# Optimization experiments

Hardware: AMD Instinct MI355X
Metric: run time of the kernel (lower is better)

Reference implementation:

```python
import jax, jax.numpy as jnp
import numpy as np
import math

DIM = 1024
NUM_HEADS = 16
QUANTUM_HEADS = 2
HEAD_DIM = DIM // NUM_HEADS          # 64
TRAD_HEADS = NUM_HEADS - QUANTUM_HEADS  # 14
B, S = 1, 1024
STEPS = 2048
LN_EPS = 1e-5


def setup_inputs() -> dict:
    key = jax.random.key(0)
    ks = jax.random.split(key, 10)
    hd2 = 2 * HEAD_DIM
    return {
        "x": jax.random.normal(ks[0], (B, S, DIM), jnp.float32),
        # to_quantum_state: Linear(head_dim -> 2*head_dim) + LayerNorm + Tanh (shared across quantum heads)
        "qs_W": jax.random.normal(ks[1], (hd2, HEAD_DIM), jnp.float32) / math.sqrt(HEAD_DIM),
        "qs_b": jnp.zeros((hd2,), jnp.float32),
        "ln_g": jnp.ones((hd2,), jnp.float32),
        "ln_b": jnp.zeros((hd2,), jnp.float32),
        # per-quantum-head scalars
        "q_freq": jax.random.normal(ks[2], (QUANTUM_HEADS,), jnp.float32) * 0.02,
        "q_shift": jax.random.normal(ks[3], (QUANTUM_HEADS,), jnp.float32) * 0.02,
        # traditional head projections (no bias)
        "Wq": jax.random.normal(ks[4], (TRAD_HEADS * HEAD_DIM, DIM), jnp.float32) / math.sqrt(DIM),
        "Wk": jax.random.normal(ks[5], (TRAD_HEADS * HEAD_DIM, DIM), jnp.float32) / math.sqrt(DIM),
        "Wv": jax.random.normal(ks[6], (TRAD_HEADS * HEAD_DIM, DIM), jnp.float32) / math.sqrt(DIM),
        # output projection (with bias)
        "Wo": jax.random.normal(ks[7], (DIM, DIM), jnp.float32) / math.sqrt(DIM),
        "bo": jnp.zeros((DIM,), jnp.float32),
    }


def _layernorm(h, g, b):
    mu = jnp.mean(h, axis=-1, keepdims=True)
    var = jnp.mean(jnp.square(h - mu), axis=-1, keepdims=True)
    return (h - mu) * jax.lax.rsqrt(var + LN_EPS) * g + b


def _forward(x, qs_W, qs_b, ln_g, ln_b, q_freq, q_shift, Wq, Wk, Wv, Wo, bo):
    cos_table = jnp.cos(jnp.linspace(0.0, 2.0 * math.pi, STEPS).astype(jnp.float32))
    scale = 1.0 / math.sqrt(HEAD_DIM)
    two_pi = 2.0 * math.pi

    outs = []
    # ---- quantum heads (small fixed loop over structurally distinct heads) ----
    for h in range(QUANTUM_HEADS):
        xh = x[..., h * HEAD_DIM:(h + 1) * HEAD_DIM]          # (B,S,hd)
        qs = jnp.tanh(_layernorm(xh @ qs_W.T + qs_b, ln_g, ln_b))  # (B,S,2hd)
        amp, phase = jnp.split(qs, 2, axis=-1)                 # each (B,S,hd)
        # per (query pos i, key pos j, feature d) phase difference
        pd = (phase[:, :, None, :] - phase[:, None, :, :]) * q_freq[h] + q_shift[h]  # (B,S,S,hd)
        idx = jnp.floor(jnp.mod(pd / two_pi * STEPS, STEPS)).astype(jnp.int32)
        interf = cos_table[idx]                                # lookup-table gather, (B,S,S,hd)
        attn = jnp.einsum('bid,bjd,bijd->bij', amp, amp, interf) * scale
        attn = jax.nn.softmax(attn, axis=-1)
        outs.append(attn @ xh)                                 # (B,S,hd), values are the raw head slice

    # ---- traditional heads: standard multi-head attention ----
    q = (x @ Wq.T).reshape(B, S, TRAD_HEADS, HEAD_DIM)
    k = (x @ Wk.T).reshape(B, S, TRAD_HEADS, HEAD_DIM)
    v = (x @ Wv.T).reshape(B, S, TRAD_HEADS, HEAD_DIM)
    scores = jnp.einsum('bqhd,bkhd->bhqk', q, k) * scale       # (B,Ht,S,S)
    probs = jax.nn.softmax(scores, axis=-1)
    trad = jnp.einsum('bhqk,bkhd->bqhd', probs, v).reshape(B, S, TRAD_HEADS * HEAD_DIM)
    outs.append(trad)

    out = jnp.concatenate(outs, axis=-1)                       # (B,S,DIM)
    return out @ Wo.T + bo


def reference(x, qs_W, qs_b, ln_g, ln_b, q_freq, q_shift, Wq, Wk, Wv, Wo, bo):
    return _forward(x, qs_W, qs_b, ln_g, ln_b, q_freq, q_shift, Wq, Wk, Wv, Wo, bo)
```

## Files before the change

### kernel.cpp

```cpp
#include <hip/hip_runtime.h>
#include <hip/hip_bf16.h>
#include <math.h>

#define DIMX 1024
#define SEQ  1024
#define HD   64
#define QH   2
#define TH   14
#define QKVN 2688
#define LN_EPS 1e-5f
#define NSPLIT 4

typedef __bf16 bf16x8 __attribute__((ext_vector_type(8)));
typedef float  f32x4  __attribute__((ext_vector_type(4)));
typedef unsigned short u16x8 __attribute__((ext_vector_type(8)));

__device__ inline unsigned short f2b_rne(float f) {
  unsigned int u = __float_as_uint(f);
  unsigned int r = (u + 0x7FFF + ((u >> 16) & 1)) >> 16;
  return (unsigned short)r;
}

__device__ inline float waveRedSum(float v) {
  #pragma unroll
  for (int off = 32; off; off >>= 1) v += __shfl_xor(v, off, 64);
  return v;
}

__global__ __launch_bounds__(256) void k_f2b_all(
    const float* __restrict__ x, const float* __restrict__ wq,
    const float* __restrict__ wk, const float* __restrict__ wv,
    const float* __restrict__ wo,
    unsigned short* __restrict__ x_bf, unsigned short* __restrict__ wqkv_bf,
    unsigned short* __restrict__ wo_bf) {
  long i = ((long)blockIdx.x * 256 + threadIdx.x) * 4;
  float4 v;
  unsigned short* dst;
  if (i < 1048576) {
    v = *reinterpret_cast<const float4*>(x + i);
    dst = x_bf + i;
  } else if (i < 3801088) {
    long j = i - 1048576;
    const float* s = (j < 917504) ? wq + j
                   : (j < 1835008) ? wk + (j - 917504)
                                   : wv + (j - 1835008);
    v = *reinterpret_cast<const float4*>(s);
    dst = wqkv_bf + j;
  } else {
    long j = i - 3801088;
    v = *reinterpret_cast<const float4*>(wo + j);
    dst = wo_bf + j;
  }
  ushort4 o;
  o.x = f2b_rne(v.x); o.y = f2b_rne(v.y); o.z = f2b_rne(v.z); o.w = f2b_rne(v.w);
  *reinterpret_cast<ushort4*>(dst) = o;
}

__global__ __launch_bounds__(128) void k_qprep(
    const float* __restrict__ x, const float* __restrict__ qsW,
    const float* __restrict__ qsb, const float* __restrict__ lng,
    const float* __restrict__ lnb, const float* __restrict__ qfreq,
    const float* __restrict__ qshift,
    unsigned short* __restrict__ qcs, unsigned short* __restrict__ kcs) {
  int b = blockIdx.x; int h = b >> 10; int i = b & 1023;
  int o = threadIdx.x;
  __shared__ float xrow[HD];
  __shared__ float red[4];
  __shared__ float qsv[128];
  if (o < HD) xrow[o] = x[i * DIMX + h * HD + o];
  __syncthreads();
  float s = qsb[o];
  #pragma unroll
  for (int d = 0; d < HD; d += 4) {
    float4 w = *reinterpret_cast<const float4*>(qsW + o * HD + d);
    float4 xv = *reinterpret_cast<const float4*>(&xrow[d]);
    s += xv.x * w.x + xv.y * w.y + xv.z * w.z + xv.w * w.w;
  }
  int wid = o >> 6, lane = o & 63;
  float ws = waveRedSum(s);
  if (lane == 0) red[wid] = ws;
  __syncthreads();
  float mu = (red[0] + red[1]) * (1.0f / 128.0f);
  float dv = s - mu;
  float ws2 = waveRedSum(dv * dv);
  if (lane == 0) red[2 + wid] = ws2;
  __syncthreads();
  float var = (red[2] + red[3]) * (1.0f / 128.0f);
  float y = dv * rsqrtf(var + LN_EPS) * lng[o] + lnb[o];
  qsv[o] = tanhf(y);
  __syncthreads();
  float freq = qfreq[h], shift = qshift[h];
  size_t base = ((size_t)h * 1024 + i) * 128;
  if (o < HD) {
    float amp = qsv[o];
    float a = qsv[64 + o] * freq + shift;
    float sn, cs;
    __sincosf(a, &sn, &cs);
    qcs[base + o]      = f2b_rne(amp * cs);
    qcs[base + 64 + o] = f2b_rne(amp * sn);
  } else {
    int d = o - 64;
    float amp = qsv[d];
    float bAng = qsv[64 + d] * freq;
    float sn, cs;
    __sincosf(bAng, &sn, &cs);
    kcs[base + d]      = f2b_rne(amp * cs);
    kcs[base + 64 + d] = f2b_rne(amp * sn);
  }
}

__global__ __launch_bounds__(256) void k_tr64(const unsigned short* __restrict__ src, int ld,
                                              int col0, unsigned short* __restrict__ dst) {
  int h = blockIdx.y, kv0 = blockIdx.x * 64;
  int t = threadIdx.x;
  __shared__ unsigned short tile[64][72];
  #pragma unroll
  for (int pass = 0; pass < 2; ++pass) {
    int s = pass * 256 + t;
    int r = s >> 3, c8 = (s & 7) * 8;
    u16x8 v = *reinterpret_cast<const u16x8*>(src + (size_t)(kv0 + r) * ld + col0 + h * 64 + c8);
    *reinterpret_cast<u16x8*>(&tile[r][c8]) = v;
  }
  __syncthreads();
  #pragma unroll
  for (int pass = 0; pass < 2; ++pass) {
    int s = pass * 256 + t;
    int d = s >> 3, k8 = (s & 7) * 8;
    u16x8 o;
    #pragma unroll
    for (int j = 0; j < 8; ++j) o[j] = tile[k8 + j][d];
    *reinterpret_cast<u16x8*>(dst + (size_t)h * 65536 + (size_t)d * 1024 + kv0 + k8) = o;
  }
}

template <int DQK>
__global__ __launch_bounds__(256) void k_fattn(
    const unsigned short* __restrict__ Qb, long q_hstep, int ldq,
    const unsigned short* __restrict__ Kb, long k_hstep, int ldk,
    const unsigned short* __restrict__ Vtb, long v_hstep, int lh0,
    float* __restrict__ pout, float* __restrict__ pml) {
  const int LQ = DQK + 8;
  const int KREG = DQK / 32;
  __shared__ unsigned short Qs[64 * LQ];
  __shared__ unsigned short Ks[2][64 * LQ];
  __shared__ unsigned short Vs[2][64 * 72];
  __shared__ unsigned short Ps[64 * 72];
  int h = blockIdx.y;
  int q0 = blockIdx.x * 64;
  int split = blockIdx.z;
  int kv0 = split * 256;
  int t = threadIdx.x, lane = t & 63, w = t >> 6;
  int g = lane >> 4, li = lane & 15;
  const unsigned short* Qp = Qb + (size_t)h * q_hstep;
  const unsigned short* Kp = Kb + (size_t)h * k_hstep;
  const unsigned short* Vp = Vtb + (size_t)h * v_hstep;

  #pragma unroll
  for (int i = 0; i < DQK / 32; ++i) {
    int s = i * 64 + lane;
    int r = s / (DQK / 8), c8 = (s % (DQK / 8)) * 8;
    u16x8 v = *reinterpret_cast<const u16x8*>(Qp + (size_t)(q0 + w * 16 + r) * ldq + c8);
    *reinterpret_cast<u16x8*>(&Qs[(w * 16 + r) * LQ + c8]) = v;
  }

  u16x8 kreg[KREG], vreg[2];
  auto loadKV = [&](int tile) {
    int j0 = kv0 + tile * 64;
    #pragma unroll
    for (int i = 0; i < KREG; ++i) {
      int s = i * 256 + t;
      int r = s / (DQK / 8), c8 = (s % (DQK / 8)) * 8;
      kreg[i] = *reinterpret_cast<const u16x8*>(Kp + (size_t)(j0 + r) * ldk + c8);
    }
    #pragma unroll
    for (int i = 0; i < 2; ++i) {
      int s = i * 256 + t;
      int d = s >> 3, c8 = (s & 7) * 8;
      vreg[i] = *reinterpret_cast<const u16x8*>(Vp + (size_t)d * 1024 + j0 + c8);
    }
  };
  auto writeKV = [&](int buf) {
    #pragma unroll
    for (int i = 0; i < KREG; ++i) {
      int s = i * 256 + t;
      int r = s / (DQK / 8), c8 = (s % (DQK / 8)) * 8;
      *reinterpret_cast<u16x8*>(&Ks[buf][r * LQ + c8]) = kreg[i];
    }
    #pragma unroll
    for (int i = 0; i < 2; ++i) {
      int s = i * 256 + t;
      int d = s >> 3, c8 = (s & 7) * 8;
      *reinterpret_cast<u16x8*>(&Vs[buf][d * 72 + c8]) = vreg[i];
    }
  };

  loadKV(0);
  writeKV(0);
  loadKV(1);
  __syncthreads();

  f32x4 acc_o[4] = {};
  float mrow[4] = {-1e30f, -1e30f, -1e30f, -1e30f};
  float lrow[4] = {0.f, 0.f, 0.f, 0.f};

  #pragma unroll
  for (int tile = 0; tile < 4; ++tile) {
    int cur = tile & 1;
    if (tile < 3) writeKV(cur ^ 1);
    if (tile < 2) loadKV(tile + 2);
    f32x4 s_acc[4] = {};
    #pragma unroll
    for (int kk = 0; kk < DQK / 32; ++kk) {
      bf16x8 aq = *reinterpret_cast<const bf16x8*>(&Qs[(w * 16 + li) * LQ + kk * 32 + g * 8]);
      #pragma unroll
      for (int n = 0; n < 4; ++n) {
        bf16x8 bk = *reinterpret_cast<const bf16x8*>(&Ks[cur][(n * 16 + li) * LQ + kk * 32 + g * 8]);
        s_acc[n] = __builtin_amdgcn_mfma_f32_16x16x32_bf16(aq, bk, s_acc[n], 0, 0, 0);
      }
    }
    #pragma unroll
    for (int r = 0; r < 4; ++r) {
      float tm = fmaxf(fmaxf(s_acc[0][r], s_acc[1][r]), fmaxf(s_acc[2][r], s_acc[3][r]));
      #pragma unroll
      for (int m = 1; m < 16; m <<= 1) tm = fmaxf(tm, __shfl_xor(tm, m, 64));
      float mn = fmaxf(mrow[r], tm);
      float sf = __expf((mrow[r] - mn) * 0.125f);
      mrow[r] = mn;
      lrow[r] *= sf;
      #pragma unroll
      for (int n = 0; n < 4; ++n) acc_o[n][r] *= sf;
      float rs = 0.f;
      #pragma unroll
      for (int n = 0; n < 4; ++n) {
        float p = __expf((s_acc[n][r] - mn) * 0.125f);
        s_acc[n][r] = p;
        rs += p;
      }
      #pragma unroll
      for (int m = 1; m < 16; m <<= 1) rs += __shfl_xor(rs, m, 64);
      lrow[r] += rs;
    }
    #pragma unroll
    for (int n = 0; n < 4; ++n)
      #pragma unroll
      for (int r = 0; r < 4; ++r)
        Ps[(w * 16 + g * 4 + r) * 72 + n * 16 + li] = f2b_rne(s_acc[n][r]);
    #pragma unroll
    for (int kk = 0; kk < 2; ++kk) {
      bf16x8 ap = *reinterpret_cast<const bf16x8*>(&Ps[(w * 16 + li) * 72 + kk * 32 + g * 8]);
      #pragma unroll
      for (int n = 0; n < 4; ++n) {
        bf16x8 bv = *reinterpret_cast<const bf16x8*>(&Vs[cur][(n * 16 + li) * 72 + kk * 32 + g * 8]);
        acc_o[n] = __builtin_amdgcn_mfma_f32_16x16x32_bf16(ap, bv, acc_o[n], 0, 0, 0);
      }
    }
    __syncthreads();
  }

  size_t rowbase = (size_t)((lh0 + h) * NSPLIT + split) * 1024;
  #pragma unroll
  for (int r = 0; r < 4; ++r) {
    int qr = q0 + w * 16 + g * 4 + r;
    #pragma unroll
    for (int n = 0; n < 4; ++n)
      pout[(rowbase + qr) * 64 + n * 16 + li] = acc_o[n][r];
    if (li == 0) {
      pml[(rowbase + qr) * 2 + 0] = mrow[r];
      pml[(rowbase + qr) * 2 + 1] = lrow[r];
    }
  }
}

__global__ __launch_bounds__(256) void k_fmerge(
    const float* __restrict__ pout, const float* __restrict__ pml,
    unsigned short* __restrict__ concat) {
  int rq = blockIdx.x * 4 + (threadIdx.x >> 6);
  int lh = rq >> 10, q = rq & 1023;
  int d = threadIdx.x & 63;
  float m_s[NSPLIT], l_s[NSPLIT];
  float M = -1e30f;
  #pragma unroll
  for (int s = 0; s < NSPLIT; ++s) {
    size_t rb = (size_t)(lh * NSPLIT + s) * 1024 + q;
    m_s[s] = pml[rb * 2 + 0];
    l_s[s] = pml[rb * 2 + 1];
    M = fmaxf(M, m_s[s]);
  }
  float num = 0.f, den = 0.f;
  #pragma unroll
  for (int s = 0; s < NSPLIT; ++s) {
    float wgt = __expf((m_s[s] - M) * 0.125f);
    num += wgt * pout[((size_t)(lh * NSPLIT + s) * 1024 + q) * 64 + d];
    den += wgt * l_s[s];
  }
  concat[(size_t)q * DIMX + lh * 64 + d] = f2b_rne(num / den);
}

template <int HAS_BIAS, int BF16_OUT>
__global__ __launch_bounds__(256) void k_bgemm(
    const unsigned short* __restrict__ A, const unsigned short* __restrict__ B,
    void* __restrict__ Cv, const float* __restrict__ bias,
    int K, int lda, int ldb, int ldc,
    long a_batch, long b_batch, long c_batch) {
  const int LDT = 72;
  __shared__ unsigned short As[64 * LDT];
  __shared__ unsigned short Bs[64 * LDT];
  int t = threadIdx.x;
  int lane = t & 63, w = t >> 6;
  int wr = w >> 1, wc = w & 1;
  int mb = blockIdx.y * 64, nb = blockIdx.x * 64;
  const unsigned short* Ab = A + (size_t)blockIdx.z * a_batch;
  const unsigned short* Bb = B + (size_t)blockIdx.z * b_batch;
  f32x4 acc[2][2] = {};
  int r0 = t >> 3;
  int c0 = (t & 7) * 8;
  for (int kb = 0; kb < K; kb += 64) {
    bf16x8 av0 = *reinterpret_cast<const bf16x8*>(Ab + (size_t)(mb + r0) * lda + kb + c0);
    bf16x8 av1 = *reinterpret_cast<const bf16x8*>(Ab + (size_t)(mb + r0 + 32) * lda + kb + c0);
    bf16x8 bv0 = *reinterpret_cast<const bf16x8*>(Bb + (size_t)(nb + r0) * ldb + kb + c0);
    bf16x8 bv1 = *reinterpret_cast<const bf16x8*>(Bb + (size_t)(nb + r0 + 32) * ldb + kb + c0);
    __syncthreads();
    *reinterpret_cast<bf16x8*>(&As[r0 * LDT + c0]) = av0;
    *reinterpret_cast<bf16x8*>(&As[(r0 + 32) * LDT + c0]) = av1;
    *reinterpret_cast<bf16x8*>(&Bs[r0 * LDT + c0]) = bv0;
    *reinterpret_cast<bf16x8*>(&Bs[(r0 + 32) * LDT + c0]) = bv1;
    __syncthreads();
    #pragma unroll
    for (int kk = 0; kk < 2; ++kk) {
      bf16x8 af[2], bfr[2];
      #pragma unroll
      for (int m = 0; m < 2; ++m)
        af[m] = *reinterpret_cast<const bf16x8*>(
            &As[(wr * 32 + m * 16 + (lane & 15)) * LDT + kk * 32 + (lane >> 4) * 8]);
      #pragma unroll
      for (int n = 0; n < 2; ++n)
        bfr[n] = *reinterpret_cast<const bf16x8*>(
            &Bs[(wc * 32 + n * 16 + (lane & 15)) * LDT + kk * 32 + (lane >> 4) * 8]);
      #pragma unroll
      for (int m = 0; m < 2; ++m)
        #pragma unroll
        for (int n = 0; n < 2; ++n)
          acc[m][n] = __builtin_amdgcn_mfma_f32_16x16x32_bf16(af[m], bfr[n], acc[m][n], 0, 0, 0);
    }
  }
  #pragma unroll
  for (int m = 0; m < 2; ++m) {
    int row0 = mb + wr * 32 + m * 16 + (lane >> 4) * 4;
    #pragma unroll
    for (int n = 0; n < 2; ++n) {
      int col = nb + wc * 32 + n * 16 + (lane & 15);
      float bval = HAS_BIAS ? bias[col] : 0.0f;
      #pragma unroll
      for (int r = 0; r < 4; ++r) {
        size_t idx = (size_t)blockIdx.z * c_batch + (size_t)(row0 + r) * ldc + col;
        if (BF16_OUT) ((unsigned short*)Cv)[idx] = f2b_rne(acc[m][n][r] + bval);
        else          ((float*)Cv)[idx] = acc[m][n][r] + bval;
      }
    }
  }
}

extern "C" void kernel_launch(void* const* d_in, const int* in_sizes, int n_in,
                              void* d_out, int out_size, void* d_ws, size_t ws_size,
                              hipStream_t stream) {
  const float* x      = (const float*)d_in[0];
  const float* qsW    = (const float*)d_in[1];
  const float* qsb    = (const float*)d_in[2];
  const float* lng    = (const float*)d_in[3];
  const float* lnb    = (const float*)d_in[4];
  const float* qfreq  = (const float*)d_in[5];
  const float* qshift = (const float*)d_in[6];
  const float* Wq     = (const float*)d_in[7];
  const float* Wk     = (const float*)d_in[8];
  const float* Wv     = (const float*)d_in[9];
  const float* Wo     = (const float*)d_in[10];
  const float* bo     = (const float*)d_in[11];
  float* out = (float*)d_out;

  char* ws = (char*)d_ws;
  size_t off = 0;
  auto alloc = [&](size_t bytes) { char* p = ws + off; off += (bytes + 255) & ~(size_t)255; return p; };
  unsigned short* x_bf      = (unsigned short*)alloc((size_t)SEQ * DIMX * 2);
  unsigned short* wqkv_bf   = (unsigned short*)alloc((size_t)QKVN * DIMX * 2);
  unsigned short* wo_bf     = (unsigned short*)alloc((size_t)DIMX * DIMX * 2);
  unsigned short* concat_bf = (unsigned short*)alloc((size_t)SEQ * DIMX * 2);
  unsigned short* qkv_bf    = (unsigned short*)alloc((size_t)SEQ * QKVN * 2);
  unsigned short* qcs       = (unsigned short*)alloc((size_t)QH * SEQ * 128 * 2);
  unsigned short* kcs       = (unsigned short*)alloc((size_t)QH * SEQ * 128 * 2);
  unsigned short* vt        = (unsigned short*)alloc((size_t)TH * HD * SEQ * 2);
  unsigned short* xt        = (unsigned short*)alloc((size_t)QH * HD * SEQ * 2);
  float*          pout      = (float*)alloc((size_t)16 * NSPLIT * SEQ * 64 * 4);
  float*          pml       = (float*)alloc((size_t)16 * NSPLIT * SEQ * 2 * 4);

  k_f2b_all<<<4736, 256, 0, stream>>>(x, Wq, Wk, Wv, Wo, x_bf, wqkv_bf, wo_bf);
  k_qprep<<<QH * SEQ, 128, 0, stream>>>(x, qsW, qsb, lng, lnb, qfreq, qshift, qcs, kcs);

  k_bgemm<0, 1><<<dim3(QKVN / 64, SEQ / 64, 1), 256, 0, stream>>>(
      x_bf, wqkv_bf, qkv_bf, nullptr, DIMX, DIMX, DIMX, QKVN, 0, 0, 0);

  k_tr64<<<dim3(16, TH), 256, 0, stream>>>(qkv_bf, QKVN, 1792, vt);
  k_tr64<<<dim3(16, QH), 256, 0, stream>>>(x_bf, DIMX, 0, xt);

  k_fattn<128><<<dim3(16, QH, NSPLIT), 256, 0, stream>>>(
      qcs, (long)SEQ * 128, 128, kcs, (long)SEQ * 128, 128, xt, (long)HD * SEQ, 0, pout, pml);
  k_fattn<64><<<dim3(16, TH, NSPLIT), 256, 0, stream>>>(
      qkv_bf, 64, QKVN, qkv_bf + 896, 64, QKVN, vt, (long)HD * SEQ, 2, pout, pml);
  k_fmerge<<<16 * SEQ / 4, 256, 0, stream>>>(pout, pml, concat_bf);

  k_bgemm<1, 0><<<dim3(DIMX / 64, SEQ / 64, 1), 256, 0, stream>>>(
      concat_bf, wo_bf, out, bo, DIMX, DIMX, DIMX, DIMX, 0, 0, 0);
}
```

Before: 86.18 us.

## Use 128x128 GEMM tiles with direct global-to-LDS loads

Replaces the 64x64 batched GEMM with a 128x128 tile kernel in which each wave computes a 4x4 grid of MFMA tiles. Operands are staged through `global_load_lds` straight into shared memory instead of going through registers. The aim is more data reuse per tile loaded and fewer instructions for each staged tile. In exchange, the grids shrink to 168 blocks for the QKV projection and 64 for the output projection, which underfills the CUs. The unpadded LDS layout may also cause bank conflicts on fragment reads.

```diff
diff --git a/kernel.cpp b/kernel.cpp
--- a/kernel.cpp
+++ b/kernel.cpp
@@ -297,62 +297,59 @@
 }
 
 template <int HAS_BIAS, int BF16_OUT>
-__global__ __launch_bounds__(256) void k_bgemm(
+__global__ __launch_bounds__(256) void k_gemm128(
     const unsigned short* __restrict__ A, const unsigned short* __restrict__ B,
     void* __restrict__ Cv, const float* __restrict__ bias,
-    int K, int lda, int ldb, int ldc,
-    long a_batch, long b_batch, long c_batch) {
-  const int LDT = 72;
-  __shared__ unsigned short As[64 * LDT];
-  __shared__ unsigned short Bs[64 * LDT];
-  int t = threadIdx.x;
-  int lane = t & 63, w = t >> 6;
+    int K, int lda, int ldb, int ldc) {
+  __shared__ unsigned short As[128 * 64];
+  __shared__ unsigned short Bs[128 * 64];
+  int t = threadIdx.x, lane = t & 63, w = t >> 6;
   int wr = w >> 1, wc = w & 1;
-  int mb = blockIdx.y * 64, nb = blockIdx.x * 64;
-  const unsigned short* Ab = A + (size_t)blockIdx.z * a_batch;
-  const unsigned short* Bb = B + (size_t)blockIdx.z * b_batch;
-  f32x4 acc[2][2] = {};
-  int r0 = t >> 3;
-  int c0 = (t & 7) * 8;
+  int g = lane >> 4, li = lane & 15;
+  int mb = blockIdx.y * 128, nb = blockIdx.x * 128;
+  int rstg = t >> 3;
+  int cstg = (t & 7) * 8;
+  f32x4 acc[4][4] = {};
   for (int kb = 0; kb < K; kb += 64) {
-    bf16x8 av0 = *reinterpret_cast<const bf16x8*>(Ab + (size_t)(mb + r0) * lda + kb + c0);
-    bf16x8 av1 = *reinterpret_cast<const bf16x8*>(Ab + (size_t)(mb + r0 + 32) * lda + kb + c0);
-    bf16x8 bv0 = *reinterpret_cast<const bf16x8*>(Bb + (size_t)(nb + r0) * ldb + kb + c0);
-    bf16x8 bv1 = *reinterpret_cast<const bf16x8*>(Bb + (size_t)(nb + r0 + 32) * ldb + kb + c0);
     __syncthreads();
-    *reinterpret_cast<bf16x8*>(&As[r0 * LDT + c0]) = av0;
-    *reinterpret_cast<bf16x8*>(&As[(r0 + 32) * LDT + c0]) = av1;
-    *reinterpret_cast<bf16x8*>(&Bs[r0 * LDT + c0]) = bv0;
-    *reinterpret_cast<bf16x8*>(&Bs[(r0 + 32) * LDT + c0]) = bv1;
+    #pragma unroll
+    for (int i = 0; i < 4; ++i) {
+      __builtin_amdgcn_global_load_lds(
+          (const __attribute__((address_space(1))) unsigned int*)(A + (size_t)(mb + i * 32 + rstg) * lda + kb + cstg),
+          (__attribute__((address_space(3))) unsigned int*)(As + (i * 256 + t) * 8),
+          16, 0, 0);
+      __builtin_amdgcn_global_load_lds(
+          (const __attribute__((address_space(1))) unsigned int*)(B + (size_t)(nb + i * 32 + rstg) * ldb + kb + cstg),
+          (__attribute__((address_space(3))) unsigned int*)(Bs + (i * 256 + t) * 8),
+          16, 0, 0);
+    }
     __syncthreads();
     #pragma unroll
     for (int kk = 0; kk < 2; ++kk) {
-      bf16x8 af[2], bfr[2];
-      #pragma unroll
-      for (int m = 0; m < 2; ++m)
-        af[m] = *reinterpret_cast<const bf16x8*>(
-            &As[(wr * 32 + m * 16 + (lane & 15)) * LDT + kk * 32 + (lane >> 4) * 8]);
-      #pragma unroll
-      for (int n = 0; n < 2; ++n)
-        bfr[n] = *reinterpret_cast<const bf16x8*>(
-            &Bs[(wc * 32 + n * 16 + (lane & 15)) * LDT + kk * 32 + (lane >> 4) * 8]);
-      #pragma unroll
-      for (int m = 0; m < 2; ++m)
+      bf16x8 af[4], bfr[4];
+      #pragma unroll
+      for (int m = 0; m < 4; ++m)
+        af[m] = *reinterpret_cast<const bf16x8*>(&As[(wr * 64 + m * 16 + li) * 64 + kk * 32 + g * 8]);
+      #pragma unroll
+      for (int n = 0; n < 4; ++n)
+        bfr[n] = *reinterpret_cast<const bf16x8*>(&Bs[(wc * 64 + n * 16 + li) * 64 + kk * 32 + g * 8]);
+      #pragma unroll
+      for (int m = 0; m < 4; ++m)
         #pragma unroll
-        for (int n = 0; n < 2; ++n)
+        for (int n = 0; n < 4; ++n)
           acc[m][n] = __builtin_amdgcn_mfma_f32_16x16x32_bf16(af[m], bfr[n], acc[m][n], 0, 0, 0);
     }
   }
   #pragma unroll
-  for (int m = 0; m < 2; ++m) {
-    int row0 = mb + wr * 32 + m * 16 + (lane >> 4) * 4;
-    #pragma unroll
-    for (int n = 0; n < 2; ++n) {
-      int col = nb + wc * 32 + n * 16 + (lane & 15);
+  for (int m = 0; m < 4; ++m) {
+    int row0 = mb + wr * 64 + m * 16 + g * 4;
+    #pragma unroll
+    for (int n = 0; n < 4; ++n) {
+      int col = nb + wc * 64 + n * 16 + li;
       float bval = HAS_BIAS ? bias[col] : 0.0f;
       #pragma unroll
       for (int r = 0; r < 4; ++r) {
-        size_t idx = (size_t)blockIdx.z * c_batch + (size_t)(row0 + r) * ldc + col;
+        size_t idx = (size_t)(row0 + r) * ldc + col;
         if (BF16_OUT) ((unsigned short*)Cv)[idx] = f2b_rne(acc[m][n][r] + bval);
         else          ((float*)Cv)[idx] = acc[m][n][r] + bval;
       }
@@ -395,8 +392,8 @@
   k_f2b_all<<<4736, 256, 0, stream>>>(x, Wq, Wk, Wv, Wo, x_bf, wqkv_bf, wo_bf);
   k_qprep<<<QH * SEQ, 128, 0, stream>>>(x, qsW, qsb, lng, lnb, qfreq, qshift, qcs, kcs);
 
-  k_bgemm<0, 1><<<dim3(QKVN / 64, SEQ / 64, 1), 256, 0, stream>>>(
-      x_bf, wqkv_bf, qkv_bf, nullptr, DIMX, DIMX, DIMX, QKVN, 0, 0, 0);
+  k_gemm128<0, 1><<<dim3(QKVN / 128, SEQ / 128), 256, 0, stream>>>(
+      x_bf, wqkv_bf, qkv_bf, nullptr, DIMX, DIMX, DIMX, QKVN);
 
   k_tr64<<<dim3(16, TH), 256, 0, stream>>>(qkv_bf, QKVN, 1792, vt);
   k_tr64<<<dim3(16, QH), 256, 0, stream>>>(x_bf, DIMX, 0, xt);
@@ -407,6 +404,6 @@
       qkv_bf, 64, QKVN, qkv_bf + 896, 64, QKVN, vt, (long)HD * SEQ, 2, pout, pml);
   k_fmerge<<<16 * SEQ / 4, 256, 0, stream>>>(pout, pml, concat_bf);
 
-  k_bgemm<1, 0><<<dim3(DIMX / 64, SEQ / 64, 1), 256, 0, stream>>>(
-      concat_bf, wo_bf, out, bo, DIMX, DIMX, DIMX, DIMX, 0, 0, 0);
-}
+  k_gemm128<1, 0><<<dim3(DIMX / 128, SEQ / 128), 256, 0, stream>>>(
+      concat_bf, wo_bf, out, bo, DIMX, DIMX, DIMX, DIMX);
+}
```

Result: slower. 105.0 us (+21.8%).
